# Performance work log

Hardware: AMD Instinct MI355X
Metric: run time of the kernel (lower is better)

The kernel has to match this reference:

```python
import jax, jax.numpy as jnp
import numpy as np

N, E, F_IN, EDGE_DIM, H, C, NUM_RELS = 20000, 160000, 64, 8, 4, 128, 4


def setup_inputs() -> dict:
    key = jax.random.key(0)
    ks = jax.random.split(key, 20)
    def rn(k, shape, s=0.05):
        return jax.random.normal(k, shape, jnp.float32) * s
    return {
        "x": rn(ks[0], (N, F_IN), 1.0),
        "edge_index": jax.random.randint(ks[1], (2, E), 0, N, dtype=jnp.int32),
        "edge_features": rn(ks[2], (E, EDGE_DIM), 1.0),
        "W1": rn(ks[3], (F_IN, H * C)), "a_src1": rn(ks[4], (H, C)), "a_dst1": rn(ks[5], (H, C)),
        "We1": rn(ks[6], (EDGE_DIM, H * C)), "a_e1": rn(ks[7], (H, C)), "b1": jnp.zeros((H * C,), jnp.float32),
        "W2": rn(ks[8], (H * C, H * C)), "a_src2": rn(ks[9], (H, C)), "a_dst2": rn(ks[10], (H, C)),
        "We2": rn(ks[11], (EDGE_DIM, H * C)), "a_e2": rn(ks[12], (H, C)), "b2": jnp.zeros((H * C,), jnp.float32),
        "Wd1": rn(ks[13], (2 * H * C, 256)), "bd1": jnp.zeros((256,), jnp.float32),
        "Wd2": rn(ks[14], (256, NUM_RELS)), "bd2": jnp.zeros((NUM_RELS,), jnp.float32),
    }


def _add_self_loops(ei, ea, n):
    # PyG add_self_loops with fill_value='mean': self-loop edge_attr is the
    # mean of incoming edge_attr per destination node (0 if no incoming edges).
    dst = ei[1]
    s = jax.ops.segment_sum(ea, dst, num_segments=n)
    cnt = jax.ops.segment_sum(jnp.ones((ea.shape[0], 1), ea.dtype), dst, num_segments=n)
    mean = s / jnp.maximum(cnt, 1.0)
    loop = jnp.arange(n, dtype=ei.dtype)
    ei2 = jnp.concatenate([ei, jnp.stack([loop, loop])], axis=1)
    ea2 = jnp.concatenate([ea, mean], axis=0)
    return ei2, ea2


def _gat_conv(x, ei, ea, W, a_s, a_d, We, a_e, b, n):
    ei, ea = _add_self_loops(ei, ea, n)
    src, dst = ei[0], ei[1]
    xp = (x @ W).reshape(n, H, C)                      # [N,H,C]
    alpha_s = jnp.einsum('nhc,hc->nh', xp, a_s)        # [N,H]
    alpha_d = jnp.einsum('nhc,hc->nh', xp, a_d)        # [N,H]
    ep = (ea @ We).reshape(-1, H, C)                   # [E',H,C]
    alpha_e = jnp.einsum('ehc,hc->eh', ep, a_e)        # [E',H]
    alpha = alpha_s[src] + alpha_d[dst] + alpha_e
    alpha = jax.nn.leaky_relu(alpha, 0.2)
    # segment softmax over edges sharing a destination node
    m = jax.ops.segment_max(alpha, dst, num_segments=n)
    ex = jnp.exp(alpha - m[dst])
    den = jax.ops.segment_sum(ex, dst, num_segments=n)
    w = ex / den[dst]                                   # [E',H]
    out = jax.ops.segment_sum(xp[src] * w[..., None], dst, num_segments=n)  # [N,H,C]
    return out.reshape(n, H * C) + b


def reference(x, edge_index, edge_features, W1, a_src1, a_dst1, We1, a_e1, b1,
              W2, a_src2, a_dst2, We2, a_e2, b2, Wd1, bd1, Wd2, bd2):
    n = x.shape[0]
    z = jax.nn.elu(_gat_conv(x, edge_index, edge_features, W1, a_src1, a_dst1, We1, a_e1, b1, n))
    z = jax.nn.elu(_gat_conv(z, edge_index, edge_features, W2, a_src2, a_dst2, We2, a_e2, b2, n))
    src, dst = edge_index[0], edge_index[1]
    rel = jnp.concatenate([z[src], z[dst]], axis=1)     # [E, 2*512]
    h = rel @ Wd1 + bd1                                 # dropout is identity at inference
    return jax.nn.sigmoid(h @ Wd2 + bd2)
```

## Files before the change

kernel.cpp:

```cpp
#include <hip/hip_runtime.h>
#include <hip/hip_bf16.h>
#include <math.h>

#define N_NODES 20000
#define N_EDGES 160000
#define FIN 64
#define EDGE_DIM 8
#define H_HEADS 4
#define C_CH 128
#define HC 512
#define NUM_RELS 4
#define E_TOT (N_EDGES + N_NODES)

typedef __bf16 bf16x8 __attribute__((ext_vector_type(8)));
typedef float f32x4 __attribute__((ext_vector_type(4)));
typedef unsigned short u16x8 __attribute__((ext_vector_type(8)));

#define NX4 (N_NODES * FIN / 4)
#define W1T (HC * FIN)
#define W2T (HC * HC)
__global__ void k_cvt(const float* __restrict__ x, __bf16* __restrict__ xb,
                      const float* __restrict__ W1, __bf16* __restrict__ Wt1,
                      const float* __restrict__ W2, __bf16* __restrict__ Wt2) {
    int tid = blockIdx.x * 256 + threadIdx.x;
    if (tid < NX4) {
        float4 v = *(const float4*)(x + (size_t)tid * 4);
        __bf16 o[4] = {(__bf16)v.x, (__bf16)v.y, (__bf16)v.z, (__bf16)v.w};
        *(ushort2*)(xb + (size_t)tid * 4) = *(ushort2*)o;
        *(ushort2*)(xb + (size_t)tid * 4 + 2) = *(ushort2*)(o + 2);
    } else if (tid < NX4 + W1T) {
        int t = tid - NX4;
        int n = t / FIN, k = t % FIN;
        Wt1[n * FIN + k] = (__bf16)W1[(size_t)k * HC + n];
    } else if (tid < NX4 + W1T + W2T) {
        int t = tid - NX4 - W1T;
        int n = t >> 9, k = t & 511;
        Wt2[n * HC + k] = (__bf16)W2[(size_t)k * HC + n];
    }
}

#define LDP 40
__global__ __launch_bounds__(256)
void k_gemm_bf16(const __bf16* __restrict__ A, const __bf16* __restrict__ Bt,
                 __bf16* __restrict__ Cb, int M, int K) {
    __shared__ __bf16 As[128 * LDP];
    __shared__ __bf16 Bs[128 * LDP];

    int nwg = gridDim.x;
    int f = blockIdx.x;
    int q = nwg >> 3, r = nwg & 7;
    int xcd = f & 7, idx = f >> 3;
    int wg = (xcd < r ? xcd * (q + 1) : r * (q + 1) + (xcd - r) * q) + idx;
    int by = wg >> 2, bx = wg & 3;
    int br = by * 128, bc = bx * 128;

    const int t = threadIdx.x;
    const int lane = t & 63;
    const int wid = t >> 6;
    const int wr = wid >> 1, wc = wid & 1;
    const int l15 = lane & 15, lkg = lane >> 4;

    const int srow = t >> 1, shalf = (t & 1) * 16;
    const int agr = br + srow;
    const __bf16* Ap = A + (size_t)agr * K + shalf;
    const __bf16* Bp = Bt + (size_t)(bc + srow) * K + shalf;

    f32x4 acc[4][4] = {};

    for (int k0 = 0; k0 < K; k0 += 32) {
        u16x8 av0 = {}, av1 = {};
        if (agr < M) {
            av0 = *(const u16x8*)(Ap + k0);
            av1 = *(const u16x8*)(Ap + k0 + 8);
        }
        u16x8 bv0 = *(const u16x8*)(Bp + k0);
        u16x8 bv1 = *(const u16x8*)(Bp + k0 + 8);
        *(u16x8*)(As + srow * LDP + shalf) = av0;
        *(u16x8*)(As + srow * LDP + shalf + 8) = av1;
        *(u16x8*)(Bs + srow * LDP + shalf) = bv0;
        *(u16x8*)(Bs + srow * LDP + shalf + 8) = bv1;
        __syncthreads();

        bf16x8 a[4], b[4];
        #pragma unroll
        for (int m = 0; m < 4; ++m)
            a[m] = *(const bf16x8*)(As + (wr * 64 + m * 16 + l15) * LDP + lkg * 8);
        #pragma unroll
        for (int n = 0; n < 4; ++n)
            b[n] = *(const bf16x8*)(Bs + (wc * 64 + n * 16 + l15) * LDP + lkg * 8);
        #pragma unroll
        for (int m = 0; m < 4; ++m)
            #pragma unroll
            for (int n = 0; n < 4; ++n)
                acc[m][n] = __builtin_amdgcn_mfma_f32_16x16x32_bf16(a[m], b[n], acc[m][n], 0, 0, 0);
        __syncthreads();
    }

    #pragma unroll
    for (int m = 0; m < 4; ++m) {
        int rbase = br + wr * 64 + m * 16 + lkg * 4;
        #pragma unroll
        for (int n = 0; n < 4; ++n) {
            int col = bc + wc * 64 + n * 16 + l15;
            #pragma unroll
            for (int rg = 0; rg < 4; ++rg) {
                int gr = rbase + rg;
                if (gr < M) Cb[(size_t)gr * HC + col] = (__bf16)acc[m][n][rg];
            }
        }
    }
}

__global__ void k_prep(const float* __restrict__ We1, const float* __restrict__ ae1,
                       const float* __restrict__ We2, const float* __restrict__ ae2,
                       float* __restrict__ q1, float* __restrict__ q2,
                       const float* __restrict__ Wd1, const float* __restrict__ Wd2,
                       const float* __restrict__ bd1, const float* __restrict__ bd2,
                       float* __restrict__ M, float* __restrict__ cvec) {
    if (blockIdx.x == 16) {
        int t = threadIdx.x;
        if (t >= 64) return;
        const float* We = (t < 32) ? We1 : We2;
        const float* ae = (t < 32) ? ae1 : ae2;
        float* q = (t < 32) ? q1 : q2;
        int i = t & 31, h = i >> 3, d = i & 7;
        float s = 0.f;
        for (int c = 0; c < 128; ++c) s += We[d * 512 + h * 128 + c] * ae[h * 128 + c];
        q[i] = s;
    } else {
        int tid = blockIdx.x * 256 + threadIdx.x;
        int i = tid >> 2, r = tid & 3;
        float s = 0.f;
        for (int k = 0; k < 256; ++k) s += Wd1[i * 256 + k] * Wd2[k * 4 + r];
        M[tid] = s;
        if (tid < 4) {
            float c = 0.f;
            for (int k = 0; k < 256; ++k) c += bd1[k] * Wd2[k * 4 + tid];
            cvec[tid] = c + bd2[tid];
        }
    }
}

__global__ void k_count(const int* __restrict__ ei, int* __restrict__ counts) {
    int e = blockIdx.x * 256 + threadIdx.x;
    if (e >= E_TOT) return;
    int dst = (e < N_EDGES) ? ei[N_EDGES + e] : (e - N_EDGES);
    atomicAdd(counts + dst, 1);
}

__global__ __launch_bounds__(1024)
void k_scan(const int* __restrict__ counts, int* __restrict__ row_start,
            int* __restrict__ nxt) {
    __shared__ int part[1024];
    int t = threadIdx.x;
    int base = t * 20;
    int pre[20];
    int s = 0;
    #pragma unroll
    for (int i = 0; i < 20; ++i) {
        int idx = base + i;
        int c = (idx < N_NODES) ? counts[idx] : 0;
        pre[i] = s; s += c;
    }
    part[t] = s;
    __syncthreads();
    for (int off = 1; off < 1024; off <<= 1) {
        int v = (t >= off) ? part[t - off] : 0;
        __syncthreads();
        part[t] += v;
        __syncthreads();
    }
    int excl = (t == 0) ? 0 : part[t - 1];
    #pragma unroll
    for (int i = 0; i < 20; ++i) {
        int idx = base + i;
        if (idx < N_NODES) { int v = excl + pre[i]; row_start[idx] = v; nxt[idx] = v; }
    }
    if (t == 1023) row_start[N_NODES] = part[1023];
}

__global__ void k_scatter(const int* __restrict__ ei, int* __restrict__ nxt,
                          int* __restrict__ csr_src, int* __restrict__ csr_eid) {
    int e = blockIdx.x * 256 + threadIdx.x;
    if (e >= E_TOT) return;
    int src, dst;
    if (e < N_EDGES) { src = ei[e]; dst = ei[N_EDGES + e]; }
    else             { src = dst = e - N_EDGES; }
    int pos = atomicAdd(nxt + dst, 1);
    csr_src[pos] = src;
    csr_eid[pos] = e;
}

__global__ void k_mean_csr(const int* __restrict__ row_start, const int* __restrict__ csr_eid,
                           const float* __restrict__ ef, float* __restrict__ meanf) {
    int n = blockIdx.x * 32 + (threadIdx.x >> 3);
    int d = threadIdx.x & 7;
    if (n >= N_NODES) return;
    int rs = row_start[n], re = row_start[n + 1];
    float s = 0.f; int c = 0;
    for (int i = rs; i < re; ++i) {
        int eid = csr_eid[i];
        if (eid < N_EDGES) { s += ef[(size_t)eid * 8 + d]; ++c; }
    }
    meanf[n * 8 + d] = s / fmaxf((float)c, 1.f);
}

__global__ __launch_bounds__(256)
void k_node_alpha(const __bf16* __restrict__ xp, const float* __restrict__ a_s,
                  const float* __restrict__ a_d, float* __restrict__ as_out,
                  float* __restrict__ ad_out) {
    int n = blockIdx.x * 4 + (threadIdx.x >> 6);
    int lane = threadIdx.x & 63;
    if (n >= N_NODES) return;
    int h = lane >> 4;
    bf16x8 xv = *(const bf16x8*)(xp + (size_t)n * HC + lane * 8);
    const float* ap = a_s + h * C_CH + (lane & 15) * 8;
    const float* dp = a_d + h * C_CH + (lane & 15) * 8;
    float4 a0 = *(const float4*)ap, a1 = *(const float4*)(ap + 4);
    float4 d0 = *(const float4*)dp, d1 = *(const float4*)(dp + 4);
    float v[8];
    #pragma unroll
    for (int k = 0; k < 8; ++k) v[k] = (float)xv[k];
    float s = v[0] * a0.x + v[1] * a0.y + v[2] * a0.z + v[3] * a0.w +
              v[4] * a1.x + v[5] * a1.y + v[6] * a1.z + v[7] * a1.w;
    float d = v[0] * d0.x + v[1] * d0.y + v[2] * d0.z + v[3] * d0.w +
              v[4] * d1.x + v[5] * d1.y + v[6] * d1.z + v[7] * d1.w;
    #pragma unroll
    for (int off = 8; off; off >>= 1) {
        s += __shfl_xor(s, off);
        d += __shfl_xor(d, off);
    }
    if ((lane & 15) == 0) {
        as_out[n * 4 + h] = s;
        ad_out[n * 4 + h] = d;
    }
}

__global__ void k_edge_ae(const int* __restrict__ ei, const float* __restrict__ ef,
                          const float* __restrict__ meanf, const float* __restrict__ q,
                          float* __restrict__ ae_all) {
    int e = blockIdx.x * 256 + threadIdx.x;
    if (e >= E_TOT) return;
    const float* fe = (e < N_EDGES) ? (ef + (size_t)e * 8)
                                    : (meanf + (size_t)(e - N_EDGES) * 8);
    float f[8];
    #pragma unroll
    for (int d = 0; d < 8; ++d) f[d] = fe[d];
    float4 o;
    float* op = &o.x;
    #pragma unroll
    for (int h = 0; h < 4; ++h) {
        float s = 0.f;
        #pragma unroll
        for (int d = 0; d < 8; ++d) s += f[d] * q[h * 8 + d];
        op[h] = s;
    }
    *(float4*)(ae_all + (size_t)e * 4) = o;
}

__device__ __forceinline__ void edge_alpha(int src, int eid, const float4 adn,
                                           const float* __restrict__ as_,
                                           const float* __restrict__ ae_all,
                                           float& a0, float& a1, float& a2, float& a3) {
    float4 asv = *(const float4*)(as_ + src * 4);
    float4 aev = *(const float4*)(ae_all + (size_t)eid * 4);
    a0 = asv.x + adn.x + aev.x; a0 = a0 > 0.f ? a0 : 0.2f * a0;
    a1 = asv.y + adn.y + aev.y; a1 = a1 > 0.f ? a1 : 0.2f * a1;
    a2 = asv.z + adn.z + aev.z; a2 = a2 > 0.f ? a2 : 0.2f * a2;
    a3 = asv.w + adn.w + aev.w; a3 = a3 > 0.f ? a3 : 0.2f * a3;
}

template <int LAYER>
__global__ __launch_bounds__(256)
void k_dst_fused(const int* __restrict__ row_start, const int* __restrict__ csr_src,
                 const int* __restrict__ csr_eid, const __bf16* __restrict__ xp,
                 const float* __restrict__ ae_all, const float* __restrict__ as_,
                 const float* __restrict__ ad_, const float* __restrict__ b,
                 __bf16* __restrict__ zb, const float* __restrict__ Mm,
                 float* __restrict__ U, float* __restrict__ V) {
    __shared__ float4 wq[4][64];
    __shared__ int    sq[4][64];
    int wv = threadIdx.x >> 6;
    int n = blockIdx.x * 4 + wv;
    int lane = threadIdx.x & 63;
    if (n >= N_NODES) return;
    int rs = row_start[n], re = row_start[n + 1];
    int cnt = re - rs;
    float4 adn = *(const float4*)(ad_ + n * 4);
    int hl = lane >> 4;

    float acc[8] = {};
    float inv;

    if (cnt <= 64) {
        float a0 = -1e30f, a1 = -1e30f, a2 = -1e30f, a3 = -1e30f;
        int src = 0;
        if (lane < cnt) {
            src = csr_src[rs + lane];
            edge_alpha(src, csr_eid[rs + lane], adn, as_, ae_all, a0, a1, a2, a3);
        }
        float m0 = a0, m1 = a1, m2 = a2, m3 = a3;
        #pragma unroll
        for (int off = 32; off; off >>= 1) {
            m0 = fmaxf(m0, __shfl_xor(m0, off));
            m1 = fmaxf(m1, __shfl_xor(m1, off));
            m2 = fmaxf(m2, __shfl_xor(m2, off));
            m3 = fmaxf(m3, __shfl_xor(m3, off));
        }
        float e0 = 0.f, e1 = 0.f, e2 = 0.f, e3 = 0.f;
        if (lane < cnt) {
            e0 = expf(a0 - m0); e1 = expf(a1 - m1);
            e2 = expf(a2 - m2); e3 = expf(a3 - m3);
        }
        wq[wv][lane] = make_float4(e0, e1, e2, e3);
        sq[wv][lane] = src;
        float d0 = e0, d1 = e1, d2 = e2, d3 = e3;
        #pragma unroll
        for (int off = 32; off; off >>= 1) {
            d0 += __shfl_xor(d0, off); d1 += __shfl_xor(d1, off);
            d2 += __shfl_xor(d2, off); d3 += __shfl_xor(d3, off);
        }
        float den = (hl == 0) ? d0 : (hl == 1) ? d1 : (hl == 2) ? d2 : d3;
        inv = 1.f / den;

        int cnt8 = (cnt + 7) & ~7;
        for (int j0 = 0; j0 < cnt8; j0 += 8) {
            bf16x8 r[8]; float w[8];
            #pragma unroll
            for (int p = 0; p < 8; ++p) {
                float4 w4 = wq[wv][j0 + p];
                int s = sq[wv][j0 + p];
                r[p] = *(const bf16x8*)(xp + (size_t)s * HC + lane * 8);
                w[p] = (hl == 0) ? w4.x : (hl == 1) ? w4.y : (hl == 2) ? w4.z : w4.w;
            }
            #pragma unroll
            for (int p = 0; p < 8; ++p)
                #pragma unroll
                for (int k = 0; k < 8; ++k) acc[k] += (float)r[p][k] * w[p];
        }
    } else {
        float m0 = -1e30f, m1 = -1e30f, m2 = -1e30f, m3 = -1e30f;
        for (int base = rs; base < re; base += 64) {
            int i = base + lane;
            if (i < re) {
                float a0, a1, a2, a3;
                edge_alpha(csr_src[i], csr_eid[i], adn, as_, ae_all, a0, a1, a2, a3);
                m0 = fmaxf(m0, a0); m1 = fmaxf(m1, a1);
                m2 = fmaxf(m2, a2); m3 = fmaxf(m3, a3);
            }
        }
        #pragma unroll
        for (int off = 32; off; off >>= 1) {
            m0 = fmaxf(m0, __shfl_xor(m0, off));
            m1 = fmaxf(m1, __shfl_xor(m1, off));
            m2 = fmaxf(m2, __shfl_xor(m2, off));
            m3 = fmaxf(m3, __shfl_xor(m3, off));
        }
        float d0 = 0.f, d1 = 0.f, d2 = 0.f, d3 = 0.f;
        for (int base = rs; base < re; base += 64) {
            int i = base + lane;
            float e0 = 0.f, e1 = 0.f, e2 = 0.f, e3 = 0.f;
            int src = 0;
            if (i < re) {
                src = csr_src[i];
                float a0, a1, a2, a3;
                edge_alpha(src, csr_eid[i], adn, as_, ae_all, a0, a1, a2, a3);
                e0 = expf(a0 - m0); e1 = expf(a1 - m1);
                e2 = expf(a2 - m2); e3 = expf(a3 - m3);
                d0 += e0; d1 += e1; d2 += e2; d3 += e3;
            }
            int cn = min(64, re - base);
            for (int j = 0; j < cn; ++j) {
                float w0 = __shfl(e0, j), w1 = __shfl(e1, j);
                float w2 = __shfl(e2, j), w3 = __shfl(e3, j);
                int sj = __shfl(src, j);
                float w = (hl == 0) ? w0 : (hl == 1) ? w1 : (hl == 2) ? w2 : w3;
                bf16x8 xv = *(const bf16x8*)(xp + (size_t)sj * HC + lane * 8);
                #pragma unroll
                for (int k = 0; k < 8; ++k) acc[k] += (float)xv[k] * w;
            }
        }
        #pragma unroll
        for (int off = 32; off; off >>= 1) {
            d0 += __shfl_xor(d0, off); d1 += __shfl_xor(d1, off);
            d2 += __shfl_xor(d2, off); d3 += __shfl_xor(d3, off);
        }
        float den = (hl == 0) ? d0 : (hl == 1) ? d1 : (hl == 2) ? d2 : d3;
        inv = 1.f / den;
    }

    float z[8];
    const float* bp = b + lane * 8;
    #pragma unroll
    for (int k = 0; k < 8; ++k) {
        float v = acc[k] * inv + bp[k];
        z[k] = (v > 0.f) ? v : expm1f(v);
    }

    if (LAYER == 1) {
        bf16x8 zv;
        #pragma unroll
        for (int k = 0; k < 8; ++k) zv[k] = (__bf16)z[k];
        *(bf16x8*)(zb + (size_t)n * HC + lane * 8) = zv;
    } else {
        float u[4] = {}, v[4] = {};
        #pragma unroll
        for (int k = 0; k < 8; ++k) {
            int fidx = lane * 8 + k;
            #pragma unroll
            for (int r = 0; r < 4; ++r) {
                u[r] += z[k] * Mm[fidx * 4 + r];
                v[r] += z[k] * Mm[(512 + fidx) * 4 + r];
            }
        }
        #pragma unroll
        for (int r = 0; r < 4; ++r) {
            #pragma unroll
            for (int off = 32; off; off >>= 1) {
                u[r] += __shfl_xor(u[r], off);
                v[r] += __shfl_xor(v[r], off);
            }
        }
        if (lane == 0) {
            #pragma unroll
            for (int r = 0; r < 4; ++r) { U[n * 4 + r] = u[r]; V[n * 4 + r] = v[r]; }
        }
    }
}

__global__ void k_edge_out(const int* __restrict__ ei, const float* __restrict__ U,
                           const float* __restrict__ V, const float* __restrict__ cvec,
                           float* __restrict__ out) {
    int idx = blockIdx.x * 256 + threadIdx.x;
    if (idx >= N_EDGES * 4) return;
    int e = idx >> 2, r = idx & 3;
    float val = U[ei[e] * 4 + r] + V[ei[N_EDGES + e] * 4 + r] + cvec[r];
    out[idx] = 1.f / (1.f + expf(-val));
}

extern "C" void kernel_launch(void* const* d_in, const int* in_sizes, int n_in,
                              void* d_out, int out_size, void* d_ws, size_t ws_size,
                              hipStream_t stream) {
    (void)in_sizes; (void)n_in; (void)out_size; (void)ws_size;
    const float* x      = (const float*)d_in[0];
    const int*   ei     = (const int*)d_in[1];
    const float* ef     = (const float*)d_in[2];
    const float* W1     = (const float*)d_in[3];
    const float* a_src1 = (const float*)d_in[4];
    const float* a_dst1 = (const float*)d_in[5];
    const float* We1    = (const float*)d_in[6];
    const float* a_e1   = (const float*)d_in[7];
    const float* b1     = (const float*)d_in[8];
    const float* W2     = (const float*)d_in[9];
    const float* a_src2 = (const float*)d_in[10];
    const float* a_dst2 = (const float*)d_in[11];
    const float* We2    = (const float*)d_in[12];
    const float* a_e2   = (const float*)d_in[13];
    const float* b2     = (const float*)d_in[14];
    const float* Wd1    = (const float*)d_in[15];
    const float* bd1    = (const float*)d_in[16];
    const float* Wd2    = (const float*)d_in[17];
    const float* bd2    = (const float*)d_in[18];
    float* out = (float*)d_out;

    float* ae_all = (float*)d_ws;
    float* as_    = ae_all + (size_t)E_TOT * 4;
    float* ad_    = as_ + N_NODES * 4;
    float* meanf  = ad_ + N_NODES * 4;
    float* q1     = meanf + N_NODES * 8;
    float* q2     = q1 + 32;
    float* Mm     = q2 + 32;
    float* cv     = Mm + 4096;
    float* U      = cv + 4;
    float* V      = U + N_NODES * 4;
    int* row_start = (int*)(V + N_NODES * 4);
    int* counts    = row_start + 20004;
    int* nxt       = counts + N_NODES;
    int* csr_src   = nxt + N_NODES;
    int* csr_eid   = csr_src + E_TOT;
    __bf16* xb   = (__bf16*)(csr_eid + E_TOT);
    __bf16* Ab   = xb + (size_t)N_NODES * FIN;
    __bf16* z1b  = Ab + (size_t)N_NODES * HC;
    __bf16* Wt1  = z1b + (size_t)N_NODES * HC;
    __bf16* Wt2  = Wt1 + HC * FIN;

    hipMemsetAsync(counts, 0, N_NODES * sizeof(int), stream);
    k_count<<<(E_TOT + 255) / 256, 256, 0, stream>>>(ei, counts);
    k_scan<<<1, 1024, 0, stream>>>(counts, row_start, nxt);
    k_scatter<<<(E_TOT + 255) / 256, 256, 0, stream>>>(ei, nxt, csr_src, csr_eid);
    k_mean_csr<<<(N_NODES + 31) / 32, 256, 0, stream>>>(row_start, csr_eid, ef, meanf);
    k_prep<<<17, 256, 0, stream>>>(We1, a_e1, We2, a_e2, q1, q2, Wd1, Wd2, bd1, bd2, Mm, cv);
    k_cvt<<<(NX4 + W1T + W2T + 255) / 256, 256, 0, stream>>>(x, xb, W1, Wt1, W2, Wt2);

    const int nwg = ((N_NODES + 127) / 128) * 4;

    k_gemm_bf16<<<nwg, 256, 0, stream>>>(xb, Wt1, Ab, N_NODES, FIN);
    k_node_alpha<<<(N_NODES + 3) / 4, 256, 0, stream>>>(Ab, a_src1, a_dst1, as_, ad_);
    k_edge_ae<<<(E_TOT + 255) / 256, 256, 0, stream>>>(ei, ef, meanf, q1, ae_all);
    k_dst_fused<1><<<(N_NODES + 3) / 4, 256, 0, stream>>>(
        row_start, csr_src, csr_eid, Ab, ae_all, as_, ad_, b1, z1b, nullptr, nullptr, nullptr);

    k_gemm_bf16<<<nwg, 256, 0, stream>>>(z1b, Wt2, Ab, N_NODES, HC);
    k_node_alpha<<<(N_NODES + 3) / 4, 256, 0, stream>>>(Ab, a_src2, a_dst2, as_, ad_);
    k_edge_ae<<<(E_TOT + 255) / 256, 256, 0, stream>>>(ei, ef, meanf, q2, ae_all);
    k_dst_fused<2><<<(N_NODES + 3) / 4, 256, 0, stream>>>(
        row_start, csr_src, csr_eid, Ab, ae_all, as_, ad_, b2, nullptr, Mm, U, V);

    k_edge_out<<<(N_EDGES * 4 + 255) / 256, 256, 0, stream>>>(ei, U, V, cv, out);
}
```

Baseline: 274.1 us.

## Split GAT softmax into CSR-ordered edge exp, per-node denominator, and gather kernels

Per-edge attention logits and exponentials are now computed in a separate kernel in CSR order, with a per-node kernel summing denominators. The gather kernel then only does weighted aggregation of source features, and it batches loads with a sched barrier. The max-subtraction in the softmax is dropped, and the output kernel is vectorized to one thread per edge with float4 I/O. This aims to remove the divergent max/sum reductions from the gather kernel and to unify its long- and short-degree paths. In exchange it adds launches and a stored csr_dst array, and it risks overflow because exp is taken without a max shift.

```diff
diff --git a/kernel.cpp b/kernel.cpp
--- a/kernel.cpp
+++ b/kernel.cpp
@@ -180,7 +180,8 @@
 }
 
 __global__ void k_scatter(const int* __restrict__ ei, int* __restrict__ nxt,
-                          int* __restrict__ csr_src, int* __restrict__ csr_eid) {
+                          int* __restrict__ csr_src, int* __restrict__ csr_eid,
+                          int* __restrict__ csr_dst) {
     int e = blockIdx.x * 256 + threadIdx.x;
     if (e >= E_TOT) return;
     int src, dst;
@@ -189,6 +190,7 @@
     int pos = atomicAdd(nxt + dst, 1);
     csr_src[pos] = src;
     csr_eid[pos] = e;
+    csr_dst[pos] = dst;
 }
 
 __global__ void k_mean_csr(const int* __restrict__ row_start, const int* __restrict__ csr_eid,
@@ -236,157 +238,90 @@
     }
 }
 
-__global__ void k_edge_ae(const int* __restrict__ ei, const float* __restrict__ ef,
+__global__ void k_edge_ex(const int* __restrict__ csr_src, const int* __restrict__ csr_dst,
+                          const int* __restrict__ csr_eid, const float* __restrict__ ef,
                           const float* __restrict__ meanf, const float* __restrict__ q,
-                          float* __restrict__ ae_all) {
-    int e = blockIdx.x * 256 + threadIdx.x;
-    if (e >= E_TOT) return;
-    const float* fe = (e < N_EDGES) ? (ef + (size_t)e * 8)
-                                    : (meanf + (size_t)(e - N_EDGES) * 8);
+                          const float* __restrict__ as_, const float* __restrict__ ad_,
+                          float* __restrict__ wbuf) {
+    int i = blockIdx.x * 256 + threadIdx.x;
+    if (i >= E_TOT) return;
+    int src = csr_src[i], dst = csr_dst[i], eid = csr_eid[i];
+    const float* fe = (eid < N_EDGES) ? (ef + (size_t)eid * 8)
+                                      : (meanf + (size_t)(eid - N_EDGES) * 8);
     float f[8];
     #pragma unroll
     for (int d = 0; d < 8; ++d) f[d] = fe[d];
+    float4 asv = *(const float4*)(as_ + src * 4);
+    float4 adv = *(const float4*)(ad_ + dst * 4);
+    const float* asp = &asv.x;
+    const float* adp = &adv.x;
     float4 o;
     float* op = &o.x;
     #pragma unroll
     for (int h = 0; h < 4; ++h) {
-        float s = 0.f;
-        #pragma unroll
-        for (int d = 0; d < 8; ++d) s += f[d] * q[h * 8 + d];
-        op[h] = s;
-    }
-    *(float4*)(ae_all + (size_t)e * 4) = o;
-}
-
-__device__ __forceinline__ void edge_alpha(int src, int eid, const float4 adn,
-                                           const float* __restrict__ as_,
-                                           const float* __restrict__ ae_all,
-                                           float& a0, float& a1, float& a2, float& a3) {
-    float4 asv = *(const float4*)(as_ + src * 4);
-    float4 aev = *(const float4*)(ae_all + (size_t)eid * 4);
-    a0 = asv.x + adn.x + aev.x; a0 = a0 > 0.f ? a0 : 0.2f * a0;
-    a1 = asv.y + adn.y + aev.y; a1 = a1 > 0.f ? a1 : 0.2f * a1;
-    a2 = asv.z + adn.z + aev.z; a2 = a2 > 0.f ? a2 : 0.2f * a2;
-    a3 = asv.w + adn.w + aev.w; a3 = a3 > 0.f ? a3 : 0.2f * a3;
+        float ae = 0.f;
+        #pragma unroll
+        for (int d = 0; d < 8; ++d) ae += f[d] * q[h * 8 + d];
+        float a = asp[h] + adp[h] + ae;
+        a = (a > 0.f) ? a : 0.2f * a;
+        op[h] = expf(a);
+    }
+    *(float4*)(wbuf + (size_t)i * 4) = o;
+}
+
+__global__ void k_den(const int* __restrict__ row_start, const float* __restrict__ wbuf,
+                      float* __restrict__ invb) {
+    int n = blockIdx.x * 256 + threadIdx.x;
+    if (n >= N_NODES) return;
+    int rs = row_start[n], re = row_start[n + 1];
+    float4 s = make_float4(0.f, 0.f, 0.f, 0.f);
+    for (int i = rs; i < re; ++i) {
+        float4 w = *(const float4*)(wbuf + (size_t)i * 4);
+        s.x += w.x; s.y += w.y; s.z += w.z; s.w += w.w;
+    }
+    float4 o = make_float4(1.f / s.x, 1.f / s.y, 1.f / s.z, 1.f / s.w);
+    *(float4*)(invb + n * 4) = o;
 }
 
 template <int LAYER>
 __global__ __launch_bounds__(256)
-void k_dst_fused(const int* __restrict__ row_start, const int* __restrict__ csr_src,
-                 const int* __restrict__ csr_eid, const __bf16* __restrict__ xp,
-                 const float* __restrict__ ae_all, const float* __restrict__ as_,
-                 const float* __restrict__ ad_, const float* __restrict__ b,
-                 __bf16* __restrict__ zb, const float* __restrict__ Mm,
-                 float* __restrict__ U, float* __restrict__ V) {
-    __shared__ float4 wq[4][64];
-    __shared__ int    sq[4][64];
+void k_gather(const int* __restrict__ row_start, const int* __restrict__ csr_src,
+              const float* __restrict__ wbuf, const float* __restrict__ invb,
+              const __bf16* __restrict__ xp, const float* __restrict__ b,
+              __bf16* __restrict__ zb, const float* __restrict__ Mm,
+              float* __restrict__ U, float* __restrict__ V) {
     int wv = threadIdx.x >> 6;
     int n = blockIdx.x * 4 + wv;
     int lane = threadIdx.x & 63;
     if (n >= N_NODES) return;
     int rs = row_start[n], re = row_start[n + 1];
     int cnt = re - rs;
-    float4 adn = *(const float4*)(ad_ + n * 4);
     int hl = lane >> 4;
+    float4 iv = *(const float4*)(invb + n * 4);
+    float inv = (hl == 0) ? iv.x : (hl == 1) ? iv.y : (hl == 2) ? iv.z : iv.w;
 
     float acc[8] = {};
-    float inv;
-
-    if (cnt <= 64) {
-        float a0 = -1e30f, a1 = -1e30f, a2 = -1e30f, a3 = -1e30f;
-        int src = 0;
-        if (lane < cnt) {
-            src = csr_src[rs + lane];
-            edge_alpha(src, csr_eid[rs + lane], adn, as_, ae_all, a0, a1, a2, a3);
-        }
-        float m0 = a0, m1 = a1, m2 = a2, m3 = a3;
-        #pragma unroll
-        for (int off = 32; off; off >>= 1) {
-            m0 = fmaxf(m0, __shfl_xor(m0, off));
-            m1 = fmaxf(m1, __shfl_xor(m1, off));
-            m2 = fmaxf(m2, __shfl_xor(m2, off));
-            m3 = fmaxf(m3, __shfl_xor(m3, off));
-        }
-        float e0 = 0.f, e1 = 0.f, e2 = 0.f, e3 = 0.f;
-        if (lane < cnt) {
-            e0 = expf(a0 - m0); e1 = expf(a1 - m1);
-            e2 = expf(a2 - m2); e3 = expf(a3 - m3);
-        }
-        wq[wv][lane] = make_float4(e0, e1, e2, e3);
-        sq[wv][lane] = src;
-        float d0 = e0, d1 = e1, d2 = e2, d3 = e3;
-        #pragma unroll
-        for (int off = 32; off; off >>= 1) {
-            d0 += __shfl_xor(d0, off); d1 += __shfl_xor(d1, off);
-            d2 += __shfl_xor(d2, off); d3 += __shfl_xor(d3, off);
-        }
-        float den = (hl == 0) ? d0 : (hl == 1) ? d1 : (hl == 2) ? d2 : d3;
-        inv = 1.f / den;
-
-        int cnt8 = (cnt + 7) & ~7;
-        for (int j0 = 0; j0 < cnt8; j0 += 8) {
-            bf16x8 r[8]; float w[8];
+    for (int c0 = 0; c0 < cnt; c0 += 64) {
+        int ccnt = min(64, cnt - c0);
+        int my_src = csr_src[rs + c0 + min(lane, ccnt - 1)];
+        for (int j0 = 0; j0 < ccnt; j0 += 8) {
+            bf16x8 rr[8];
+            float wl[8];
             #pragma unroll
             for (int p = 0; p < 8; ++p) {
-                float4 w4 = wq[wv][j0 + p];
-                int s = sq[wv][j0 + p];
-                r[p] = *(const bf16x8*)(xp + (size_t)s * HC + lane * 8);
-                w[p] = (hl == 0) ? w4.x : (hl == 1) ? w4.y : (hl == 2) ? w4.z : w4.w;
+                int sp = __shfl(my_src, j0 + p);
+                int slot = rs + c0 + min(j0 + p, ccnt - 1);
+                wl[p] = wbuf[(size_t)slot * 4 + hl];
+                rr[p] = *(const bf16x8*)(xp + (size_t)sp * HC + lane * 8);
             }
-            #pragma unroll
-            for (int p = 0; p < 8; ++p)
+            __builtin_amdgcn_sched_barrier(0);
+            #pragma unroll
+            for (int p = 0; p < 8; ++p) {
+                float wp = (j0 + p < ccnt) ? wl[p] : 0.f;
                 #pragma unroll
-                for (int k = 0; k < 8; ++k) acc[k] += (float)r[p][k] * w[p];
-        }
-    } else {
-        float m0 = -1e30f, m1 = -1e30f, m2 = -1e30f, m3 = -1e30f;
-        for (int base = rs; base < re; base += 64) {
-            int i = base + lane;
-            if (i < re) {
-                float a0, a1, a2, a3;
-                edge_alpha(csr_src[i], csr_eid[i], adn, as_, ae_all, a0, a1, a2, a3);
-                m0 = fmaxf(m0, a0); m1 = fmaxf(m1, a1);
-                m2 = fmaxf(m2, a2); m3 = fmaxf(m3, a3);
+                for (int k = 0; k < 8; ++k) acc[k] += (float)rr[p][k] * wp;
             }
         }
-        #pragma unroll
-        for (int off = 32; off; off >>= 1) {
-            m0 = fmaxf(m0, __shfl_xor(m0, off));
-            m1 = fmaxf(m1, __shfl_xor(m1, off));
-            m2 = fmaxf(m2, __shfl_xor(m2, off));
-            m3 = fmaxf(m3, __shfl_xor(m3, off));
-        }
-        float d0 = 0.f, d1 = 0.f, d2 = 0.f, d3 = 0.f;
-        for (int base = rs; base < re; base += 64) {
-            int i = base + lane;
-            float e0 = 0.f, e1 = 0.f, e2 = 0.f, e3 = 0.f;
-            int src = 0;
-            if (i < re) {
-                src = csr_src[i];
-                float a0, a1, a2, a3;
-                edge_alpha(src, csr_eid[i], adn, as_, ae_all, a0, a1, a2, a3);
-                e0 = expf(a0 - m0); e1 = expf(a1 - m1);
-                e2 = expf(a2 - m2); e3 = expf(a3 - m3);
-                d0 += e0; d1 += e1; d2 += e2; d3 += e3;
-            }
-            int cn = min(64, re - base);
-            for (int j = 0; j < cn; ++j) {
-                float w0 = __shfl(e0, j), w1 = __shfl(e1, j);
-                float w2 = __shfl(e2, j), w3 = __shfl(e3, j);
-                int sj = __shfl(src, j);
-                float w = (hl == 0) ? w0 : (hl == 1) ? w1 : (hl == 2) ? w2 : w3;
-                bf16x8 xv = *(const bf16x8*)(xp + (size_t)sj * HC + lane * 8);
-                #pragma unroll
-                for (int k = 0; k < 8; ++k) acc[k] += (float)xv[k] * w;
-            }
-        }
-        #pragma unroll
-        for (int off = 32; off; off >>= 1) {
-            d0 += __shfl_xor(d0, off); d1 += __shfl_xor(d1, off);
-            d2 += __shfl_xor(d2, off); d3 += __shfl_xor(d3, off);
-        }
-        float den = (hl == 0) ? d0 : (hl == 1) ? d1 : (hl == 2) ? d2 : d3;
-        inv = 1.f / den;
     }
 
     float z[8];
@@ -431,11 +366,17 @@
 __global__ void k_edge_out(const int* __restrict__ ei, const float* __restrict__ U,
                            const float* __restrict__ V, const float* __restrict__ cvec,
                            float* __restrict__ out) {
-    int idx = blockIdx.x * 256 + threadIdx.x;
-    if (idx >= N_EDGES * 4) return;
-    int e = idx >> 2, r = idx & 3;
-    float val = U[ei[e] * 4 + r] + V[ei[N_EDGES + e] * 4 + r] + cvec[r];
-    out[idx] = 1.f / (1.f + expf(-val));
+    int e = blockIdx.x * 256 + threadIdx.x;
+    if (e >= N_EDGES) return;
+    float4 u = *(const float4*)(U + (size_t)ei[e] * 4);
+    float4 v = *(const float4*)(V + (size_t)ei[N_EDGES + e] * 4);
+    float4 c = *(const float4*)cvec;
+    float4 o;
+    o.x = 1.f / (1.f + expf(-(u.x + v.x + c.x)));
+    o.y = 1.f / (1.f + expf(-(u.y + v.y + c.y)));
+    o.z = 1.f / (1.f + expf(-(u.z + v.z + c.z)));
+    o.w = 1.f / (1.f + expf(-(u.w + v.w + c.w)));
+    *(float4*)(out + (size_t)e * 4) = o;
 }
 
 extern "C" void kernel_launch(void* const* d_in, const int* in_sizes, int n_in,
@@ -463,10 +404,11 @@
     const float* bd2    = (const float*)d_in[18];
     float* out = (float*)d_out;
 
-    float* ae_all = (float*)d_ws;
-    float* as_    = ae_all + (size_t)E_TOT * 4;
+    float* wbuf   = (float*)d_ws;
+    float* as_    = wbuf + (size_t)E_TOT * 4;
     float* ad_    = as_ + N_NODES * 4;
-    float* meanf  = ad_ + N_NODES * 4;
+    float* invb   = ad_ + N_NODES * 4;
+    float* meanf  = invb + N_NODES * 4;
     float* q1     = meanf + N_NODES * 8;
     float* q2     = q1 + 32;
     float* Mm     = q2 + 32;
@@ -478,7 +420,8 @@
     int* nxt       = counts + N_NODES;
     int* csr_src   = nxt + N_NODES;
     int* csr_eid   = csr_src + E_TOT;
-    __bf16* xb   = (__bf16*)(csr_eid + E_TOT);
+    int* csr_dst   = csr_eid + E_TOT;
+    __bf16* xb   = (__bf16*)(csr_dst + E_TOT);
     __bf16* Ab   = xb + (size_t)N_NODES * FIN;
     __bf16* z1b  = Ab + (size_t)N_NODES * HC;
     __bf16* Wt1  = z1b + (size_t)N_NODES * HC;
@@ -487,24 +430,29 @@
     hipMemsetAsync(counts, 0, N_NODES * sizeof(int), stream);
     k_count<<<(E_TOT + 255) / 256, 256, 0, stream>>>(ei, counts);
     k_scan<<<1, 1024, 0, stream>>>(counts, row_start, nxt);
-    k_scatter<<<(E_TOT + 255) / 256, 256, 0, stream>>>(ei, nxt, csr_src, csr_eid);
+    k_scatter<<<(E_TOT + 255) / 256, 256, 0, stream>>>(ei, nxt, csr_src, csr_eid, csr_dst);
     k_mean_csr<<<(N_NODES + 31) / 32, 256, 0, stream>>>(row_start, csr_eid, ef, meanf);
     k_prep<<<17, 256, 0, stream>>>(We1, a_e1, We2, a_e2, q1, q2, Wd1, Wd2, bd1, bd2, Mm, cv);
     k_cvt<<<(NX4 + W1T + W2T + 255) / 256, 256, 0, stream>>>(x, xb, W1, Wt1, W2, Wt2);
 
     const int nwg = ((N_NODES + 127) / 128) * 4;
+    const int nblk = (N_NODES + 3) / 4;
 
     k_gemm_bf16<<<nwg, 256, 0, stream>>>(xb, Wt1, Ab, N_NODES, FIN);
-    k_node_alpha<<<(N_NODES + 3) / 4, 256, 0, stream>>>(Ab, a_src1, a_dst1, as_, ad_);
-    k_edge_ae<<<(E_TOT + 255) / 256, 256, 0, stream>>>(ei, ef, meanf, q1, ae_all);
-    k_dst_fused<1><<<(N_NODES + 3) / 4, 256, 0, stream>>>(
-        row_start, csr_src, csr_eid, Ab, ae_all, as_, ad_, b1, z1b, nullptr, nullptr, nullptr);
+    k_node_alpha<<<nblk, 256, 0, stream>>>(Ab, a_src1, a_dst1, as_, ad_);
+    k_edge_ex<<<(E_TOT + 255) / 256, 256, 0, stream>>>(csr_src, csr_dst, csr_eid, ef, meanf,
+                                                       q1, as_, ad_, wbuf);
+    k_den<<<(N_NODES + 255) / 256, 256, 0, stream>>>(row_start, wbuf, invb);
+    k_gather<1><<<nblk, 256, 0, stream>>>(row_start, csr_src, wbuf, invb, Ab, b1,
+                                          z1b, nullptr, nullptr, nullptr);
 
     k_gemm_bf16<<<nwg, 256, 0, stream>>>(z1b, Wt2, Ab, N_NODES, HC);
-    k_node_alpha<<<(N_NODES + 3) / 4, 256, 0, stream>>>(Ab, a_src2, a_dst2, as_, ad_);
-    k_edge_ae<<<(E_TOT + 255) / 256, 256, 0, stream>>>(ei, ef, meanf, q2, ae_all);
-    k_dst_fused<2><<<(N_NODES + 3) / 4, 256, 0, stream>>>(
-        row_start, csr_src, csr_eid, Ab, ae_all, as_, ad_, b2, nullptr, Mm, U, V);
-
-    k_edge_out<<<(N_EDGES * 4 + 255) / 256, 256, 0, stream>>>(ei, U, V, cv, out);
-}
+    k_node_alpha<<<nblk, 256, 0, stream>>>(Ab, a_src2, a_dst2, as_, ad_);
+    k_edge_ex<<<(E_TOT + 255) / 256, 256, 0, stream>>>(csr_src, csr_dst, csr_eid, ef, meanf,
+                                                       q2, as_, ad_, wbuf);
+    k_den<<<(N_NODES + 255) / 256, 256, 0, stream>>>(row_start, wbuf, invb);
+    k_gather<2><<<nblk, 256, 0, stream>>>(row_start, csr_src, wbuf, invb, Ab, b2,
+                                          nullptr, Mm, U, V);
+
+    k_edge_out<<<(N_EDGES + 255) / 256, 256, 0, stream>>>(ei, U, V, cv, out);
+}
```

Result: slower. 282.3 us (+3.0%).
